# Kernel tuning notes

Hardware: AMD Instinct MI355X
Metric: run time of the kernel (lower is better)

## Reference

```python
import jax, jax.numpy as jnp
import numpy as np

N = 100000      # nodes
E = 1600000     # edges (avg degree 16)
IN = 64         # in_feats
OUT = 64        # out_feats per head
H = 4           # heads
SLOPE = 0.2     # leaky relu negative slope


def setup_inputs() -> dict:
    key = jax.random.key(0)
    ks = jax.random.split(key, 6)
    feat = jax.random.normal(ks[0], (N, IN), dtype=jnp.float32)
    # xavier-ish scale for weights
    W_weight = jax.random.normal(ks[1], (OUT * H, IN), dtype=jnp.float32) * (2.0 / (IN + OUT * H)) ** 0.5
    W_bias = jnp.zeros((OUT * H,), dtype=jnp.float32)
    a_l = jax.random.normal(ks[2], (1, OUT, H), dtype=jnp.float32) * 0.1
    a_r = jax.random.normal(ks[3], (1, OUT, H), dtype=jnp.float32) * 0.1
    row = jax.random.randint(ks[4], (E,), 0, N, dtype=jnp.int32)
    col = jax.random.randint(ks[5], (E,), 0, N, dtype=jnp.int32)
    return {"feat": feat, "W_weight": W_weight, "W_bias": W_bias,
            "a_l": a_l, "a_r": a_r, "row": row, "col": col}


def reference(feat, W_weight, W_bias, a_l, a_r, row, col):
    n = feat.shape[0]
    # linear projection -> [N, OUT, H]
    Z = (feat @ W_weight.T + W_bias).reshape(n, OUT, H)
    # per-node attention logits [N, H]
    e_l = (Z * a_l).sum(axis=1)
    e_r = (Z * a_r).sum(axis=1)
    # edge scores + leaky relu [E, H]
    e = e_l[row] + e_r[col]
    a = jnp.where(e > 0, e, SLOPE * e)
    # segment softmax over incoming edges of each destination row
    m = jax.ops.segment_max(a, row, num_segments=n)          # [N, H]
    ex = jnp.exp(a - m[row])                                  # [E, H]
    s = jax.ops.segment_sum(ex, row, num_segments=n)          # [N, H]
    alpha = ex / s[row]                                       # [E, H]
    # weighted aggregation: out[i,:,h] = sum_{e: row[e]=i} alpha[e,h] * Z[col[e],:,h]
    msg = alpha[:, None, :] * Z[col]                          # [E, OUT, H]
    out = jax.ops.segment_sum(msg, row, num_segments=n)       # [N, OUT, H]
    return out.reshape(n, -1)
```

## Files before the change

### kernel.cpp

```cpp
#include <hip/hip_runtime.h>
#include <stdint.h>

#define SLOPE  0.2f
#define PN     64
#define CAP    48
#define NXCD   8

typedef float    f32x4 __attribute__((ext_vector_type(4)));
typedef _Float16 h16x2 __attribute__((ext_vector_type(2)));

union FU { float f; unsigned int u; };
union HU { unsigned int u; h16x2 h; };
__device__ __forceinline__ float ubits(unsigned int u) { FU c; c.u = u; return c.f; }

__global__ __launch_bounds__(256) void front_kernel(
    const int* __restrict__ row, const int* __restrict__ col,
    int* __restrict__ cnt, int* __restrict__ csr,
    const float4* __restrict__ feat4, const float* __restrict__ W,
    const float* __restrict__ bias, const float* __restrict__ a_l,
    const float* __restrict__ a_r,
    uint2* __restrict__ featb2, float* __restrict__ el, float* __restrict__ er,
    unsigned int* __restrict__ WtHu, float* __restrict__ biasP,
    int E, int rng, int N, int SC, int PJ)
{
    __shared__ float fT[64][68];
    __shared__ float WlS[8][68];
    __shared__ float blS[8];

    int b = blockIdx.x;
    int t = threadIdx.x;

    if (b < SC) {
        int xcd = b & (NXCD - 1);
        int chunk = b >> 3;
        int rlo = xcd * rng;
        int rhi = min(rlo + rng, N);
        int base = chunk * 1024 + t;
        #pragma unroll
        for (int q = 0; q < 4; q++) {
            int e = base + q * 256;
            if (e < E) {
                int r = __builtin_nontemporal_load(&row[e]);
                if (r >= rlo && r < rhi) {
                    int pos = atomicAdd(&cnt[r], 1);
                    if (pos < CAP)
                        csr[r * CAP + pos] = __builtin_nontemporal_load(&col[e]);
                }
            }
        }
        return;
    }
    if (b < SC + PJ) {
        int nodeBase = (b - SC) * PN;

        for (int p = t; p < PN * 16; p += 256) {
            int n = p >> 4, kq = p & 15;
            int gn = nodeBase + n;
            float4 v = make_float4(0.f, 0.f, 0.f, 0.f);
            if (gn < N) v = feat4[(size_t)gn * 16 + kq];
            fT[kq * 4 + 0][n] = v.x; fT[kq * 4 + 1][n] = v.y;
            fT[kq * 4 + 2][n] = v.z; fT[kq * 4 + 3][n] = v.w;
            if (gn < N) {
                HU u0, u1;
                u0.h = (h16x2){ (_Float16)v.x, (_Float16)v.y };
                u1.h = (h16x2){ (_Float16)v.z, (_Float16)v.w };
                featb2[(size_t)gn * 16 + kq] = make_uint2(u0.u, u1.u);
            }
        }
        for (int r = 0; r < 2; r++) {
            int id = t + 256 * r;
            int x = id >> 6, k = id & 63, h = x & 3;
            const float* v = (x < 4) ? a_l : a_r;
            float s = 0.f;
            for (int d = 0; d < 64; d++) {
                int o = d * 4 + h;
                s += v[o] * W[o * 64 + k];
            }
            WlS[x][k] = s;
        }
        if (t < 8) {
            int h = t & 3;
            const float* v = (t < 4) ? a_l : a_r;
            float s = 0.f;
            for (int d = 0; d < 64; d++) { int o = d * 4 + h; s += v[o] * bias[o]; }
            blS[t] = s;
        }
        __syncthreads();

        for (int r = 0; r < 2; r++) {
            int id = t + 256 * r;
            int n = id >> 3, x = id & 7;
            int gn = nodeBase + n;
            if (gn < N) {
                float e = blS[x];
                #pragma unroll 8
                for (int k = 0; k < 64; k++) e += fT[k][n] * WlS[x][k];
                if (x < 4) el[(size_t)gn * 4 + x] = e;
                else       er[(size_t)gn * 4 + (x - 4)] = e;
            }
        }
        return;
    }
    if (b < SC + PJ + 32) {
        int g = (b - SC - PJ) * 256 + t;
        int kk = g >> 8, cp = g & 255;
        int o = (cp & 63) * 4 + (cp >> 6);
        HU u;
        u.h = (h16x2){ (_Float16)W[o * 64 + 2 * kk], (_Float16)W[o * 64 + 2 * kk + 1] };
        WtHu[kk * 256 + cp] = u.u;
        return;
    }
    {
        int cp = t;
        int o = (cp & 63) * 4 + (cp >> 6);
        biasP[cp] = bias[o];
    }
}

__global__ __launch_bounds__(256) void gat_aggregate(
    const uint2* __restrict__ featb2,
    const float* __restrict__ el, const float* __restrict__ er,
    const int* __restrict__ cnt, const int* __restrict__ csr,
    uint2* __restrict__ agg, int N, int rng)
{
    __shared__ float aL[4][64];
    __shared__ int   cL[4][16];

    int t = threadIdx.x, lane = t & 63, w = t >> 6;
    int xcd = blockIdx.x & (NXCD - 1);
    int j = blockIdx.x >> 3;
    int local = j * 4 + w;
    int i = xcd * rng + local;
    if (local >= rng || i >= N) return;

    int start = i * CAP;
    int dg = min(cnt[i], CAP);
    int eL = lane >> 2, hh = lane & 3;
    int hsel = lane >> 4, kq = lane & 15;
    float elh = el[i * 4 + hh];

    float m = -3.0e38f;
    float m_h = -3.0e38f;
    float l = 0.f;
    float a0 = 0.f, a1 = 0.f, a2 = 0.f, a3 = 0.f;

    int c = 0;
    if (eL < dg) c = csr[start + eL];

    for (int base = 0; base < dg; base += 16) {
        int cnt2 = min(16, dg - base);
        bool full = (cnt2 > 8);

        if (hh == 0) cL[w][eL] = c;

        float ev = er[c * 4 + hh];

        uint2 fq[16];
        #pragma unroll
        for (int jj = 0; jj < 2; jj++) {
            int4 c4 = *(const int4*)&cL[w][4 * jj];
            fq[4 * jj + 0] = featb2[(unsigned)(c4.x * 16 + kq)];
            fq[4 * jj + 1] = featb2[(unsigned)(c4.y * 16 + kq)];
            fq[4 * jj + 2] = featb2[(unsigned)(c4.z * 16 + kq)];
            fq[4 * jj + 3] = featb2[(unsigned)(c4.w * 16 + kq)];
        }
        if (full) {
            #pragma unroll
            for (int jj = 2; jj < 4; jj++) {
                int4 c4 = *(const int4*)&cL[w][4 * jj];
                fq[4 * jj + 0] = featb2[(unsigned)(c4.x * 16 + kq)];
                fq[4 * jj + 1] = featb2[(unsigned)(c4.y * 16 + kq)];
                fq[4 * jj + 2] = featb2[(unsigned)(c4.z * 16 + kq)];
                fq[4 * jj + 3] = featb2[(unsigned)(c4.w * 16 + kq)];
            }
        }

        int rem = dg - base - 16;
        int cn = 0;
        if (rem > 0 && eL < rem) cn = csr[start + base + 16 + eL];

        float e  = elh + ev;
        float sc = (eL < cnt2) ? (e > 0.f ? e : SLOPE * e) : -3.0e38f;
        float v = sc;
        v = fmaxf(v, __shfl_xor(v, 4));
        v = fmaxf(v, __shfl_xor(v, 8));
        v = fmaxf(v, __shfl_xor(v, 16));
        v = fmaxf(v, __shfl_xor(v, 32));
        float mnew = fmaxf(m, v);
        float a = __expf(sc - mnew);
        float sv = a;
        sv += __shfl_xor(sv, 4);
        sv += __shfl_xor(sv, 8);
        sv += __shfl_xor(sv, 16);
        sv += __shfl_xor(sv, 32);
        l = l * __expf(m - mnew) + sv;
        m = mnew;

        aL[w][hh * 16 + eL] = a;

        float mn_h = __shfl(mnew, hsel);
        float r = __expf(m_h - mn_h);
        a0 *= r; a1 *= r; a2 *= r; a3 *= r;
        m_h = mn_h;

        #pragma unroll
        for (int jj = 0; jj < 2; jj++) {
            f32x4 al4 = *(const f32x4*)&aL[w][hsel * 16 + 4 * jj];
            #pragma unroll
            for (int q = 0; q < 4; q++) {
                float al = al4[q];
                HU hx, hy; hx.u = fq[4 * jj + q].x; hy.u = fq[4 * jj + q].y;
                a0 += al * (float)hx.h[0];
                a1 += al * (float)hx.h[1];
                a2 += al * (float)hy.h[0];
                a3 += al * (float)hy.h[1];
            }
        }
        if (full) {
            #pragma unroll
            for (int jj = 2; jj < 4; jj++) {
                f32x4 al4 = *(const f32x4*)&aL[w][hsel * 16 + 4 * jj];
                #pragma unroll
                for (int q = 0; q < 4; q++) {
                    float al = al4[q];
                    HU hx, hy; hx.u = fq[4 * jj + q].x; hy.u = fq[4 * jj + q].y;
                    a0 += al * (float)hx.h[0];
                    a1 += al * (float)hx.h[1];
                    a2 += al * (float)hy.h[0];
                    a3 += al * (float)hy.h[1];
                }
            }
        }
        c = cn;
    }

    float lh  = __shfl(l, hsel);
    float inv = (lh > 0.f) ? 1.0f / lh : 0.f;
    HU p0, p1;
    p0.h = (h16x2){ (_Float16)(a0 * inv), (_Float16)(a1 * inv) };
    p1.h = (h16x2){ (_Float16)(a2 * inv), (_Float16)(a3 * inv) };
    agg[(unsigned)(i * 64 + lane)] = make_uint2(p0.u, p1.u);
}

__global__ __launch_bounds__(256) void gemm_kernel(
    const uint4* __restrict__ agg4,
    const uint4* __restrict__ WtH4,
    const float* __restrict__ biasP,
    const int* __restrict__ cnt,
    float* __restrict__ out, int N)
{
    __shared__ char smem[32768 + 17408 + 128];
    unsigned int* WtS   = (unsigned int*)smem;
    unsigned int* aggSu = (unsigned int*)(smem + 32768);
    int*          cntS  = (int*)(smem + 32768 + 17408);
    float*        obS   = (float*)smem;

    int t = threadIdx.x;
    int nodeBase = blockIdx.x * 32;

    #pragma unroll
    for (int p = 0; p < 8; p++)
        *(uint4*)&WtS[(p * 256 + t) * 4] = WtH4[p * 256 + t];
    for (int p = t; p < 1024; p += 256) {
        int n = p >> 5, q = p & 31;
        int gn = nodeBase + n;
        uint4 v = make_uint4(0u, 0u, 0u, 0u);
        if (gn < N) v = agg4[(size_t)gn * 32 + q];
        *(uint4*)&aggSu[n * 132 + q * 4] = v;
    }
    if (t < 32) { int gn = nodeBase + t; cntS[t] = (gn < N) ? cnt[gn] : 0; }
    __syncthreads();

    int cg = t & 31, ng = t >> 5;
    int h = cg >> 3;
    float acc[4][8];
    #pragma unroll
    for (int u = 0; u < 4; u++)
        #pragma unroll
        for (int j = 0; j < 8; j++) acc[u][j] = 0.f;

    for (int kk = 0; kk < 32; kk++) {
        uint4 wv0 = *(const uint4*)&WtS[kk * 256 + cg * 8];
        uint4 wv1 = *(const uint4*)&WtS[kk * 256 + cg * 8 + 4];
        unsigned int au[4];
        #pragma unroll
        for (int u = 0; u < 4; u++)
            au[u] = aggSu[(ng * 4 + u) * 132 + h * 32 + kk];
        HU wp[8];
        wp[0].u = wv0.x; wp[1].u = wv0.y; wp[2].u = wv0.z; wp[3].u = wv0.w;
        wp[4].u = wv1.x; wp[5].u = wv1.y; wp[6].u = wv1.z; wp[7].u = wv1.w;
        #pragma unroll
        for (int u = 0; u < 4; u++) {
            HU av; av.u = au[u];
            #pragma unroll
            for (int j = 0; j < 8; j++)
                acc[u][j] = __builtin_amdgcn_fdot2(av.h, wp[j].h, acc[u][j], false);
        }
    }

    float4 b0 = *(const float4*)&biasP[cg * 8];
    float4 b1 = *(const float4*)&biasP[cg * 8 + 4];
    float bj[8] = { b0.x, b0.y, b0.z, b0.w, b1.x, b1.y, b1.z, b1.w };
    int bq[4];
    #pragma unroll
    for (int u = 0; u < 4; u++) bq[u] = cntS[ng * 4 + u];
    __syncthreads();

    #pragma unroll
    for (int u = 0; u < 4; u++) {
        int n = ng * 4 + u;
        float bsc = (bq[u] > 0) ? 1.f : 0.f;
        f32x4 x0 = { acc[u][0] + bsc * bj[0], acc[u][1] + bsc * bj[1],
                     acc[u][2] + bsc * bj[2], acc[u][3] + bsc * bj[3] };
        f32x4 x1 = { acc[u][4] + bsc * bj[4], acc[u][5] + bsc * bj[5],
                     acc[u][6] + bsc * bj[6], acc[u][7] + bsc * bj[7] };
        *(f32x4*)&obS[n * 264 + cg * 8]     = x0;
        *(f32x4*)&obS[n * 264 + cg * 8 + 4] = x1;
    }
    __syncthreads();

    int ln = t >> 3, part = t & 7;
    int gn = nodeBase + ln;
    if (gn < N) {
        #pragma unroll
        for (int k = 0; k < 8; k++) {
            int d = k * 8 + part;
            f32x4 o4 = { obS[ln * 264 +   0 + d], obS[ln * 264 +  64 + d],
                         obS[ln * 264 + 128 + d], obS[ln * 264 + 192 + d] };
            __builtin_nontemporal_store(o4, (f32x4*)(out + (size_t)gn * 256) + d);
        }
    }
}

extern "C" void kernel_launch(void* const* d_in, const int* in_sizes, int n_in,
                              void* d_out, int out_size, void* d_ws, size_t ws_size,
                              hipStream_t stream)
{
    const float* feat  = (const float*)d_in[0];
    const float* W     = (const float*)d_in[1];
    const float* bias  = (const float*)d_in[2];
    const float* a_l   = (const float*)d_in[3];
    const float* a_r   = (const float*)d_in[4];
    const int*   row   = (const int*)d_in[5];
    const int*   col   = (const int*)d_in[6];
    float* out = (float*)d_out;

    int N = in_sizes[0] / 64;
    int E = in_sizes[5];

    char* ws = (char*)d_ws;
    size_t off = 0;
    auto alloc = [&](size_t bytes) -> void* {
        void* p = (void*)(ws + off);
        off += (bytes + 255) & ~(size_t)255;
        return p;
    };
    unsigned short* featb = (unsigned short*)alloc((size_t)N * 64 * sizeof(unsigned short));
    unsigned int*   WtHu  = (unsigned int*)alloc(8192 * sizeof(unsigned int));
    float*          biasP = (float*)alloc(256 * sizeof(float));
    float* el    = (float*)alloc((size_t)N * 4 * sizeof(float));
    float* er    = (float*)alloc((size_t)N * 4 * sizeof(float));
    int*   cnt   = (int*)alloc((size_t)N * sizeof(int));
    int*   csr   = (int*)alloc((size_t)N * CAP * sizeof(int));
    uint2* agg   = (uint2*)alloc((size_t)N * 64 * sizeof(uint2));
    (void)ws_size; (void)n_in; (void)out_size;

    int rng = (N + NXCD - 1) / NXCD;
    int EC  = (E + 1023) / 1024;
    int SC  = EC * NXCD;
    int PJ  = (N + PN - 1) / PN;
    int GB  = (rng + 3) / 4;

    hipMemsetAsync(cnt, 0, (size_t)N * sizeof(int), stream);
    front_kernel<<<SC + PJ + 33, 256, 0, stream>>>(
        row, col, cnt, csr, (const float4*)feat, W, bias, a_l, a_r,
        (uint2*)featb, el, er, WtHu, biasP, E, rng, N, SC, PJ);
    gat_aggregate<<<GB * NXCD, 256, 0, stream>>>(
        (const uint2*)featb, el, er, cnt, csr, agg, N, rng);
    gemm_kernel<<<(N + 31) / 32, 256, 0, stream>>>(
        (const uint4*)agg, (const uint4*)WtHu, biasP, cnt, out, N);
}
```

Measured before the change: 337.7 us.

## Bucket edges by 64-node blocks and build per-node lists in shared memory

Result: slower. 677.2 us (+100.5%).

```diff
diff --git a/kernel.cpp b/kernel.cpp
--- a/kernel.cpp
+++ b/kernel.cpp
@@ -4,6 +4,8 @@
 #define SLOPE  0.2f
 #define PN     64
 #define CAP    48
+#define BCAP   1280
+#define PSH    20
 #define NXCD   8
 
 typedef float    f32x4 __attribute__((ext_vector_type(4)));
@@ -15,7 +17,7 @@
 
 __global__ __launch_bounds__(256) void front_kernel(
     const int* __restrict__ row, const int* __restrict__ col,
-    int* __restrict__ cnt, int* __restrict__ csr,
+    int* __restrict__ bcnt, unsigned int* __restrict__ bucket,
     const float4* __restrict__ feat4, const float* __restrict__ W,
     const float* __restrict__ bias, const float* __restrict__ a_l,
     const float* __restrict__ a_r,
@@ -42,9 +44,12 @@
             if (e < E) {
                 int r = __builtin_nontemporal_load(&row[e]);
                 if (r >= rlo && r < rhi) {
-                    int pos = atomicAdd(&cnt[r], 1);
-                    if (pos < CAP)
-                        csr[r * CAP + pos] = __builtin_nontemporal_load(&col[e]);
+                    int bk = r >> 6;
+                    int pos = atomicAdd(&bcnt[bk], 1);
+                    if (pos < BCAP)
+                        bucket[(size_t)bk * BCAP + pos] =
+                            (unsigned)__builtin_nontemporal_load(&col[e]) |
+                            ((unsigned)(r & 63) << PSH);
                 }
             }
         }
@@ -120,105 +125,102 @@
 __global__ __launch_bounds__(256) void gat_aggregate(
     const uint2* __restrict__ featb2,
     const float* __restrict__ el, const float* __restrict__ er,
-    const int* __restrict__ cnt, const int* __restrict__ csr,
-    uint2* __restrict__ agg, int N, int rng)
+    const int* __restrict__ bcnt, const unsigned int* __restrict__ bucket,
+    uint2* __restrict__ agg, int* __restrict__ deg,
+    int N, int bpx, int NB)
 {
-    __shared__ float aL[4][64];
-    __shared__ int   cL[4][16];
+    __shared__ int      cntL[64];
+    __shared__ unsigned listL[64 * CAP];
+    __shared__ float    aL[4][64];
 
     int t = threadIdx.x, lane = t & 63, w = t >> 6;
     int xcd = blockIdx.x & (NXCD - 1);
-    int j = blockIdx.x >> 3;
-    int local = j * 4 + w;
-    int i = xcd * rng + local;
-    if (local >= rng || i >= N) return;
-
-    int start = i * CAP;
-    int dg = min(cnt[i], CAP);
+    int jb = blockIdx.x >> 3;
+    int bk = xcd * bpx + jb;
+    if (bk >= NB) return;
+    int nodeBase = bk << 6;
+
+    for (int p = t; p < 64 * CAP / 4; p += 256)
+        *(uint4*)&listL[p * 4] = make_uint4(0u, 0u, 0u, 0u);
+    if (t < 64) cntL[t] = 0;
+    __syncthreads();
+
+    int ec = min(bcnt[bk], BCAP);
+    for (int p = t; p < ec; p += 256) {
+        unsigned wd = bucket[(size_t)bk * BCAP + p];
+        int nl = wd >> PSH;
+        int pos = atomicAdd(&cntL[nl], 1);
+        if (pos < CAP) listL[nl * CAP + pos] = wd & ((1u << PSH) - 1);
+    }
+    __syncthreads();
+
     int eL = lane >> 2, hh = lane & 3;
     int hsel = lane >> 4, kq = lane & 15;
-    float elh = el[i * 4 + hh];
-
-    float m = -3.0e38f;
-    float m_h = -3.0e38f;
-    float l = 0.f;
-    float a0 = 0.f, a1 = 0.f, a2 = 0.f, a3 = 0.f;
-
-    int c = 0;
-    if (eL < dg) c = csr[start + eL];
-
-    for (int base = 0; base < dg; base += 16) {
-        int cnt2 = min(16, dg - base);
-        bool full = (cnt2 > 8);
-
-        if (hh == 0) cL[w][eL] = c;
-
-        float ev = er[c * 4 + hh];
-
-        uint2 fq[16];
-        #pragma unroll
-        for (int jj = 0; jj < 2; jj++) {
-            int4 c4 = *(const int4*)&cL[w][4 * jj];
-            fq[4 * jj + 0] = featb2[(unsigned)(c4.x * 16 + kq)];
-            fq[4 * jj + 1] = featb2[(unsigned)(c4.y * 16 + kq)];
-            fq[4 * jj + 2] = featb2[(unsigned)(c4.z * 16 + kq)];
-            fq[4 * jj + 3] = featb2[(unsigned)(c4.w * 16 + kq)];
-        }
-        if (full) {
+
+    for (int u = 0; u < 16; u++) {
+        int nl = w * 16 + u;
+        int i = nodeBase + nl;
+        if (i >= N) break;
+        int dg = min(cntL[nl], CAP);
+        const unsigned* lst = &listL[nl * CAP];
+        float elh = el[i * 4 + hh];
+
+        float m = -3.0e38f, m_h = -3.0e38f, l = 0.f;
+        float a0 = 0.f, a1 = 0.f, a2 = 0.f, a3 = 0.f;
+
+        for (int base = 0; base < dg; base += 16) {
+            int cnt2 = min(16, dg - base);
+            bool full = (cnt2 > 8);
+
+            int c = (eL < cnt2) ? (int)lst[base + eL] : 0;
+            float ev = er[c * 4 + hh];
+
+            uint2 fq[16];
             #pragma unroll
-            for (int jj = 2; jj < 4; jj++) {
-                int4 c4 = *(const int4*)&cL[w][4 * jj];
-                fq[4 * jj + 0] = featb2[(unsigned)(c4.x * 16 + kq)];
-                fq[4 * jj + 1] = featb2[(unsigned)(c4.y * 16 + kq)];
-                fq[4 * jj + 2] = featb2[(unsigned)(c4.z * 16 + kq)];
-                fq[4 * jj + 3] = featb2[(unsigned)(c4.w * 16 + kq)];
-            }
-        }
-
-        int rem = dg - base - 16;
-        int cn = 0;
-        if (rem > 0 && eL < rem) cn = csr[start + base + 16 + eL];
-
-        float e  = elh + ev;
-        float sc = (eL < cnt2) ? (e > 0.f ? e : SLOPE * e) : -3.0e38f;
-        float v = sc;
-        v = fmaxf(v, __shfl_xor(v, 4));
-        v = fmaxf(v, __shfl_xor(v, 8));
-        v = fmaxf(v, __shfl_xor(v, 16));
-        v = fmaxf(v, __shfl_xor(v, 32));
-        float mnew = fmaxf(m, v);
-        float a = __expf(sc - mnew);
-        float sv = a;
-        sv += __shfl_xor(sv, 4);
-        sv += __shfl_xor(sv, 8);
-        sv += __shfl_xor(sv, 16);
-        sv += __shfl_xor(sv, 32);
-        l = l * __expf(m - mnew) + sv;
-        m = mnew;
-
-        aL[w][hh * 16 + eL] = a;
-
-        float mn_h = __shfl(mnew, hsel);
-        float r = __expf(m_h - mn_h);
-        a0 *= r; a1 *= r; a2 *= r; a3 *= r;
-        m_h = mn_h;
-
-        #pragma unroll
-        for (int jj = 0; jj < 2; jj++) {
-            f32x4 al4 = *(const f32x4*)&aL[w][hsel * 16 + 4 * jj];
+            for (int jj = 0; jj < 2; jj++) {
+                uint4 c4 = *(const uint4*)&lst[base + 4 * jj];
+                fq[4 * jj + 0] = featb2[c4.x * 16 + kq];
+                fq[4 * jj + 1] = featb2[c4.y * 16 + kq];
+                fq[4 * jj + 2] = featb2[c4.z * 16 + kq];
+                fq[4 * jj + 3] = featb2[c4.w * 16 + kq];
+            }
+            if (full) {
+                #pragma unroll
+                for (int jj = 2; jj < 4; jj++) {
+                    uint4 c4 = *(const uint4*)&lst[base + 4 * jj];
+                    fq[4 * jj + 0] = featb2[c4.x * 16 + kq];
+                    fq[4 * jj + 1] = featb2[c4.y * 16 + kq];
+                    fq[4 * jj + 2] = featb2[c4.z * 16 + kq];
+                    fq[4 * jj + 3] = featb2[c4.w * 16 + kq];
+                }
+            }
+
+            float e  = elh + ev;
+            float sc = (eL < cnt2) ? (e > 0.f ? e : SLOPE * e) : -3.0e38f;
+            float v = sc;
+            v = fmaxf(v, __shfl_xor(v, 4));
+            v = fmaxf(v, __shfl_xor(v, 8));
+            v = fmaxf(v, __shfl_xor(v, 16));
+            v = fmaxf(v, __shfl_xor(v, 32));
+            float mnew = fmaxf(m, v);
+            float a = __expf(sc - mnew);
+            float sv = a;
+            sv += __shfl_xor(sv, 4);
+            sv += __shfl_xor(sv, 8);
+            sv += __shfl_xor(sv, 16);
+            sv += __shfl_xor(sv, 32);
+            l = l * __expf(m - mnew) + sv;
+            m = mnew;
+
+            aL[w][hh * 16 + eL] = a;
+
+            float mn_h = __shfl(mnew, hsel);
+            float r = __expf(m_h - mn_h);
+            a0 *= r; a1 *= r; a2 *= r; a3 *= r;
+            m_h = mn_h;
+
             #pragma unroll
-            for (int q = 0; q < 4; q++) {
-                float al = al4[q];
-                HU hx, hy; hx.u = fq[4 * jj + q].x; hy.u = fq[4 * jj + q].y;
-                a0 += al * (float)hx.h[0];
-                a1 += al * (float)hx.h[1];
-                a2 += al * (float)hy.h[0];
-                a3 += al * (float)hy.h[1];
-            }
-        }
-        if (full) {
-            #pragma unroll
-            for (int jj = 2; jj < 4; jj++) {
+            for (int jj = 0; jj < 2; jj++) {
                 f32x4 al4 = *(const f32x4*)&aL[w][hsel * 16 + 4 * jj];
                 #pragma unroll
                 for (int q = 0; q < 4; q++) {
@@ -230,29 +232,49 @@
                     a3 += al * (float)hy.h[1];
                 }
             }
-        }
-        c = cn;
-    }
-
-    float lh  = __shfl(l, hsel);
-    float inv = (lh > 0.f) ? 1.0f / lh : 0.f;
-    HU p0, p1;
-    p0.h = (h16x2){ (_Float16)(a0 * inv), (_Float16)(a1 * inv) };
-    p1.h = (h16x2){ (_Float16)(a2 * inv), (_Float16)(a3 * inv) };
-    agg[(unsigned)(i * 64 + lane)] = make_uint2(p0.u, p1.u);
+            if (full) {
+                #pragma unroll
+                for (int jj = 2; jj < 4; jj++) {
+                    f32x4 al4 = *(const f32x4*)&aL[w][hsel * 16 + 4 * jj];
+                    #pragma unroll
+                    for (int q = 0; q < 4; q++) {
+                        float al = al4[q];
+                        HU hx, hy; hx.u = fq[4 * jj + q].x; hy.u = fq[4 * jj + q].y;
+                        a0 += al * (float)hx.h[0];
+                        a1 += al * (float)hx.h[1];
+                        a2 += al * (float)hy.h[0];
+                        a3 += al * (float)hy.h[1];
+                    }
+                }
+            }
+        }
+
+        float lh  = __shfl(l, hsel);
+        float inv = (lh > 0.f) ? 1.0f / lh : 0.f;
+        HU p0, p1;
+        p0.h = (h16x2){ (_Float16)(a0 * inv), (_Float16)(a1 * inv) };
+        p1.h = (h16x2){ (_Float16)(a2 * inv), (_Float16)(a3 * inv) };
+        agg[(unsigned)(i * 64 + lane)] = make_uint2(p0.u, p1.u);
+    }
+
+    __syncthreads();
+    if (t < 64) {
+        int i = nodeBase + t;
+        if (i < N) deg[i] = min(cntL[t], CAP);
+    }
 }
 
 __global__ __launch_bounds__(256) void gemm_kernel(
     const uint4* __restrict__ agg4,
     const uint4* __restrict__ WtH4,
     const float* __restrict__ biasP,
-    const int* __restrict__ cnt,
+    const int* __restrict__ deg,
     float* __restrict__ out, int N)
 {
     __shared__ char smem[32768 + 17408 + 128];
     unsigned int* WtS   = (unsigned int*)smem;
     unsigned int* aggSu = (unsigned int*)(smem + 32768);
-    int*          cntS  = (int*)(smem + 32768 + 17408);
+    int*          degS  = (int*)(smem + 32768 + 17408);
     float*        obS   = (float*)smem;
 
     int t = threadIdx.x;
@@ -268,7 +290,7 @@
         if (gn < N) v = agg4[(size_t)gn * 32 + q];
         *(uint4*)&aggSu[n * 132 + q * 4] = v;
     }
-    if (t < 32) { int gn = nodeBase + t; cntS[t] = (gn < N) ? cnt[gn] : 0; }
+    if (t < 32) { int gn = nodeBase + t; degS[t] = (gn < N) ? deg[gn] : 0; }
     __syncthreads();
 
     int cg = t & 31, ng = t >> 5;
@@ -303,7 +325,7 @@
     float bj[8] = { b0.x, b0.y, b0.z, b0.w, b1.x, b1.y, b1.z, b1.w };
     int bq[4];
     #pragma unroll
-    for (int u = 0; u < 4; u++) bq[u] = cntS[ng * 4 + u];
+    for (int u = 0; u < 4; u++) bq[u] = degS[ng * 4 + u];
     __syncthreads();
 
     #pragma unroll
@@ -355,28 +377,31 @@
         off += (bytes + 255) & ~(size_t)255;
         return p;
     };
+    int NB  = (N + 63) >> 6;
+    int bpx = (NB + NXCD - 1) / NXCD;
+    int rng = bpx * 64;
+
     unsigned short* featb = (unsigned short*)alloc((size_t)N * 64 * sizeof(unsigned short));
     unsigned int*   WtHu  = (unsigned int*)alloc(8192 * sizeof(unsigned int));
     float*          biasP = (float*)alloc(256 * sizeof(float));
-    float* el    = (float*)alloc((size_t)N * 4 * sizeof(float));
-    float* er    = (float*)alloc((size_t)N * 4 * sizeof(float));
-    int*   cnt   = (int*)alloc((size_t)N * sizeof(int));
-    int*   csr   = (int*)alloc((size_t)N * CAP * sizeof(int));
-    uint2* agg   = (uint2*)alloc((size_t)N * 64 * sizeof(uint2));
+    float* el     = (float*)alloc((size_t)N * 4 * sizeof(float));
+    float* er     = (float*)alloc((size_t)N * 4 * sizeof(float));
+    int*   bcnt   = (int*)alloc((size_t)NB * sizeof(int));
+    unsigned int* bucket = (unsigned int*)alloc((size_t)NB * BCAP * sizeof(unsigned int));
+    uint2* agg    = (uint2*)alloc((size_t)N * 64 * sizeof(uint2));
+    int*   deg    = (int*)alloc((size_t)N * sizeof(int));
     (void)ws_size; (void)n_in; (void)out_size;
 
-    int rng = (N + NXCD - 1) / NXCD;
     int EC  = (E + 1023) / 1024;
     int SC  = EC * NXCD;
     int PJ  = (N + PN - 1) / PN;
-    int GB  = (rng + 3) / 4;
-
-    hipMemsetAsync(cnt, 0, (size_t)N * sizeof(int), stream);
+
+    hipMemsetAsync(bcnt, 0, (size_t)NB * sizeof(int), stream);
     front_kernel<<<SC + PJ + 33, 256, 0, stream>>>(
-        row, col, cnt, csr, (const float4*)feat, W, bias, a_l, a_r,
+        row, col, bcnt, bucket, (const float4*)feat, W, bias, a_l, a_r,
         (uint2*)featb, el, er, WtHu, biasP, E, rng, N, SC, PJ);
-    gat_aggregate<<<GB * NXCD, 256, 0, stream>>>(
-        (const uint2*)featb, el, er, cnt, csr, agg, N, rng);
+    gat_aggregate<<<bpx * NXCD, 256, 0, stream>>>(
+        (const uint2*)featb, el, er, bcnt, bucket, agg, deg, N, bpx, NB);
     gemm_kernel<<<(N + 31) / 32, 256, 0, stream>>>(
-        (const uint4*)agg, (const uint4*)WtHu, biasP, cnt, out, N);
+        (const uint4*)agg, (const uint4*)WtHu, biasP, deg, out, N);
 }
```
